# Performance work log

Measured on AMD Instinct MI355X. Metric: run time of the kernel, lower is better.

The kernel has to match this reference:

```python
import jax, jax.numpy as jnp
import numpy as np

B, T, V, E, H = 4096, 16, 512, 512, 1024


def setup_inputs() -> dict:
    key = jax.random.key(0)
    ks = jax.random.split(key, 8)
    s = 0.05  # weight init scale
    return {
        "encoded_input": jax.random.normal(ks[0], (B, H), jnp.float32),
        "target": jax.random.randint(ks[1], (B, T), 0, V, jnp.int32),
        "emb": jax.random.normal(ks[2], (V, E), jnp.float32) * s,
        "W_ih": jax.random.normal(ks[3], (4 * H, E), jnp.float32) * s,
        "W_hh": jax.random.normal(ks[4], (4 * H, H), jnp.float32) * s,
        "b_ih": jax.random.normal(ks[5], (4 * H,), jnp.float32) * s,
        "b_hh": jax.random.normal(ks[6], (4 * H,), jnp.float32) * s,
        "W_out": jax.random.normal(ks[7], (V, H), jnp.float32) * s,
    }


def reference(encoded_input, target, emb, W_ih, W_hh, b_ih, b_hh, W_out):
    # Teacher-forced char LSTM decoder. Dropout(0.1) is identity in eval mode.
    b, t = target.shape
    # input char ids: start token 0, then shifted targets
    inp_ids = jnp.concatenate(
        [jnp.zeros((b, 1), target.dtype), target[:, :-1]], axis=1)  # [B,T]
    x = emb[inp_ids]  # [B,T,E]
    # precompute input contribution to gates for all steps
    xg = jnp.einsum('bte,ge->btg', x, W_ih) + b_ih + b_hh  # [B,T,4H]

    def step(carry, xs):
        h, c = carry
        xg_t, tgt_t = xs  # [B,4H], [B]
        gates = xg_t + h @ W_hh.T  # [B,4H]
        i, f, g, o = jnp.split(gates, 4, axis=-1)  # torch order i,f,g,o
        i = jax.nn.sigmoid(i)
        f = jax.nn.sigmoid(f)
        g = jnp.tanh(g)
        o = jax.nn.sigmoid(o)
        c = f * c + i * g
        h = o * jnp.tanh(c)
        logits = h @ W_out.T  # [B,V]
        # NLL of log_softmax at target index, expressed stably
        lse = jax.nn.logsumexp(logits, axis=-1)
        tgt_logit = jnp.take_along_axis(logits, tgt_t[:, None], axis=1)[:, 0]
        loss_t = lse - tgt_logit  # [B]
        return (h, c), loss_t

    h0 = encoded_input  # hidden = (encoded, encoded) for 1 layer
    (_, _), losses = jax.lax.scan(
        step, (h0, h0),
        (jnp.swapaxes(xg, 0, 1), target.T))  # scan over time: [T,B,...]
    return losses.sum(axis=0) / t  # [B] per-example mean loss
```

## Files before the change

kernel.cpp:

```cpp
#include <hip/hip_runtime.h>
#include <hip/hip_bf16.h>
#include <stdint.h>

typedef __attribute__((ext_vector_type(8))) short bf16x8;
typedef __attribute__((ext_vector_type(4))) float f32x4;

#define DEV __device__ __forceinline__
#define MFMA16(a, b, c) __builtin_amdgcn_mfma_f32_16x16x32_bf16(a, b, c, 0, 0, 0)

static constexpr int Bn = 4096;
static constexpr int Tn = 16;
static constexpr int Vn = 512;
static constexpr int En = 512;
static constexpr int Hn = 1024;
static constexpr int G4 = 4096;

DEV unsigned short f2bf(float f) {
    union { float f; uint32_t u; } v; v.f = f;
    return (unsigned short)((v.u + 0x7fffu + ((v.u >> 16) & 1u)) >> 16);
}
DEV float bf2f(unsigned short h) {
    union { uint32_t u; float f; } v; v.u = (uint32_t)h << 16; return v.f;
}
DEV float sigmoidf_(float x) { return 1.f / (1.f + __expf(-x)); }
DEV float tanhf_(float x)    { return 1.f - 2.f / (1.f + __expf(2.f * x)); }

DEV bf16x8 cvt8(const float* p) {
    f32x4 a = *(const f32x4*)p;
    f32x4 b = *(const f32x4*)(p + 4);
    bf16x8 o;
    o[0] = (short)f2bf(a[0]); o[1] = (short)f2bf(a[1]);
    o[2] = (short)f2bf(a[2]); o[3] = (short)f2bf(a[3]);
    o[4] = (short)f2bf(b[0]); o[5] = (short)f2bf(b[1]);
    o[6] = (short)f2bf(b[2]); o[7] = (short)f2bf(b[3]);
    return o;
}

#define GLOAD16(s, d) __builtin_amdgcn_global_load_lds( \
    (const __attribute__((address_space(1))) uint32_t*)(s), \
    (__attribute__((address_space(3))) uint32_t*)(d), 16, 0, 0)

__launch_bounds__(1024, 4)
__global__ void lstm8(const unsigned short* __restrict__ Whp8,
                      const unsigned short* __restrict__ Hin,
                      const unsigned short* __restrict__ EGb,
                      const int* __restrict__ target, int t,
                      unsigned short* __restrict__ CstF,
                      unsigned short* __restrict__ Hout)
{
    __shared__ __align__(16) unsigned short lds[65536];

    const int tid = threadIdx.x;
    const int l   = tid & 63;
    const int w   = tid >> 6;
    const int wm  = w >> 2, wn = w & 3;
    const int q   = l >> 4, c15 = l & 15;
    const int bx  = blockIdx.x, by = blockIdx.y;
    const int n0  = bx * 256;
    const int U0  = by * 64;

    const int cBt = (((tid & 7) ^ ((tid >> 3) & 7)) << 3);
    const int sw0   = ((q ^ (c15 & 7)) << 3);
    const int offA0 = wm * 4096 + c15 * 64 + sw0;
    const int offB0 = wn * 4096 + c15 * 64 + sw0;

    f32x4 acc[4][4];
#pragma unroll
    for (int i = 0; i < 4; i++)
#pragma unroll
        for (int j = 0; j < 4; j++) acc[i][j] = f32x4{0.f, 0.f, 0.f, 0.f};

    auto stA = [&](int kts, int cbuf) {
        const unsigned short* page =
            Whp8 + (((size_t)(by * 16 + kts) * 2) << 13);
#pragma unroll
        for (int h = 0; h < 2; h++)
            GLOAD16(page + h * 8192 + tid * 8,
                    &lds[cbuf * 16384 + h * 8192 + tid * 8]);
    };
    auto stB = [&](int kts, int cbuf) {
#pragma unroll
        for (int h = 0; h < 2; h++)
            GLOAD16(Hin + (size_t)(n0 + h * 128 + (tid >> 3)) * Hn
                        + kts * 64 + cBt,
                    &lds[32768 + cbuf * 16384 + h * 8192 + tid * 8]);
    };

    stA(0, 0); stB(0, 0);
    stA(1, 1); stB(1, 1);
    asm volatile("s_waitcnt vmcnt(4)" ::: "memory");
    __builtin_amdgcn_s_barrier();

#pragma unroll 2
    for (int kt = 0; kt < 16; kt++) {
        const int cur = kt & 1;
        const unsigned short* Ab = &lds[cur * 16384];
        const unsigned short* Bb = &lds[32768 + cur * 16384];
        bf16x8 aF[4], bF[4];

#pragma unroll
        for (int i = 0; i < 4; i++)
            aF[i] = *(const bf16x8*)&Ab[offA0 + i * 1024];
#pragma unroll
        for (int j = 0; j < 4; j++)
            bF[j] = *(const bf16x8*)&Bb[offB0 + j * 1024];
        __builtin_amdgcn_s_setprio(1);
#pragma unroll
        for (int i = 0; i < 4; i++)
#pragma unroll
            for (int j = 0; j < 4; j++)
                acc[i][j] = MFMA16(aF[i], bF[j], acc[i][j]);
        __builtin_amdgcn_s_setprio(0);

#pragma unroll
        for (int i = 0; i < 4; i++)
            aF[i] = *(const bf16x8*)&Ab[(offA0 ^ 32) + i * 1024];
#pragma unroll
        for (int j = 0; j < 4; j++)
            bF[j] = *(const bf16x8*)&Bb[(offB0 ^ 32) + j * 1024];
        __builtin_amdgcn_s_setprio(1);
#pragma unroll
        for (int i = 0; i < 4; i++)
#pragma unroll
            for (int j = 0; j < 4; j++)
                acc[i][j] = MFMA16(aF[i], bF[j], acc[i][j]);
        __builtin_amdgcn_s_setprio(0);
        __builtin_amdgcn_s_barrier();

        const int kts = (kt + 2 < 16) ? (kt + 2) : 15;
        stA(kts, cur);
        stB(kts, cur);
        asm volatile("s_waitcnt vmcnt(4)" ::: "memory");
        __builtin_amdgcn_s_barrier();
    }

    int ids[4];
#pragma unroll
    for (int j = 0; j < 4; j++)
        ids[j] = (t > 0)
            ? target[(size_t)(n0 + wn * 64 + j * 16 + c15) * Tn + (t - 1)] : 0;

    unsigned short* sH = &lds[32768];
#pragma unroll
    for (int i = 0; i < 4; i++) {
        const int Uloc = wm * 16 + i * 4 + q;
#pragma unroll
        for (int j = 0; j < 4; j++) {
            uint2 egu = *(const uint2*)&EGb[(size_t)ids[j] * G4 + (U0 + Uloc) * 4];
            float e0 = bf2f((unsigned short)(egu.x & 0xffffu));
            float e1 = bf2f((unsigned short)(egu.x >> 16));
            float e2 = bf2f((unsigned short)(egu.y & 0xffffu));
            float e3 = bf2f((unsigned short)(egu.y >> 16));
            float ig = sigmoidf_(acc[i][j][0] + e0);
            float fg = sigmoidf_(acc[i][j][1] + e1);
            float gg = tanhf_  (acc[i][j][2] + e2);
            float og = sigmoidf_(acc[i][j][3] + e3);
            const size_t cidx =
                ((((size_t)(by * 16 + bx) * 16 + w) * 16 + i * 4 + j) << 6) + l;
            float cOld = bf2f(CstF[cidx]);
            float cNew = fg * cOld + ig * gg;
            float h    = og * tanhf_(cNew);
            CstF[cidx] = f2bf(cNew);
            const int bl = wn * 64 + j * 16 + c15;
            sH[bl * 64 + (Uloc ^ ((bl & 7) << 3))] = f2bf(h);
        }
    }
    __syncthreads();
    {
        const int row  = tid >> 2;
        const int part = tid & 3;
        size_t go = (size_t)(n0 + row) * Hn + U0;
#pragma unroll
        for (int s = 0; s < 2; s++) {
            const int slog = part * 2 + s;
            bf16x8 v = *(const bf16x8*)&sH[row * 64 + ((slog ^ (row & 7)) << 3)];
            *(bf16x8*)&Hout[go + slog * 8] = v;
        }
    }
}

__launch_bounds__(512, 1)
__global__ void logits256(const unsigned short* __restrict__ A,
                          const unsigned short* __restrict__ Wob,
                          const int* __restrict__ target,
                          float* __restrict__ partS,
                          float* __restrict__ partT)
{
    __shared__ __align__(16) unsigned short lds[65536];
    __shared__ float redS[4 * 256];
    __shared__ float redT[4 * 256];
    __shared__ int   tgL[256];

    const int tid = threadIdx.x;
    const int l   = tid & 63;
    const int w   = tid >> 6;
    const int wm  = w >> 2, wn = w & 3;
    const int q   = l >> 4, c15 = l & 15;
    const int bid = blockIdx.x;
    const int rb  = bid & 255, cb = bid >> 8;
    const int r0  = rb * 256;
    const int v0  = cb * 256;

    if (tid < 256) {
        int ra = r0 + tid;
        tgL[tid] = target[(size_t)(ra & (Bn - 1)) * Tn + (ra >> 12)];
    }

    const int cB    = (((l & 7) ^ (l >> 3)) << 3);
    const int sw0   = ((q ^ (c15 & 7)) << 3);
    const int offA0 = c15 * 64 + sw0;
    const int offB0 = ((wn & 1) * 64 + c15) * 64 + sw0;

    f32x4 acc[8][4];
#pragma unroll
    for (int i = 0; i < 8; i++)
#pragma unroll
        for (int j = 0; j < 4; j++) acc[i][j] = f32x4{0.f, 0.f, 0.f, 0.f};

    auto stA = [&](int kts, int cbuf) {
#pragma unroll
        for (int h = 0; h < 2; h++)
#pragma unroll
            for (int L = 0; L < 2; L++)
                GLOAD16(A + (size_t)(r0 + h * 128 + L * 64 + w * 8 + (l >> 3)) * Hn
                            + kts * 64 + cB,
                        &lds[cbuf * 16384 + h * 8192 + L * 4096 + w * 512]);
    };
    auto stB = [&](int kts, int cbuf) {
#pragma unroll
        for (int h = 0; h < 2; h++)
#pragma unroll
            for (int L = 0; L < 2; L++)
                GLOAD16(Wob + (size_t)(v0 + h * 128 + L * 64 + w * 8 + (l >> 3)) * Hn
                            + kts * 64 + cB,
                        &lds[32768 + cbuf * 16384 + h * 8192 + L * 4096 + w * 512]);
    };

    stA(0, 0); stB(0, 0);
    stA(1, 1); stB(1, 1);
    asm volatile("s_waitcnt vmcnt(8)" ::: "memory");
    __builtin_amdgcn_s_barrier();

#pragma unroll 2
    for (int kt = 0; kt < 16; kt++) {
        const int cur = kt & 1;
        const unsigned short* Ab = &lds[cur * 16384 + wm * 8192];
        const unsigned short* Bb = &lds[32768 + cur * 16384 + (wn >> 1) * 8192];
        bf16x8 aF[8], bF[4];

#pragma unroll
        for (int i = 0; i < 8; i++)
            aF[i] = *(const bf16x8*)&Ab[offA0 + i * 1024];
#pragma unroll
        for (int j = 0; j < 4; j++)
            bF[j] = *(const bf16x8*)&Bb[offB0 + j * 1024];
        __builtin_amdgcn_s_setprio(1);
#pragma unroll
        for (int i = 0; i < 8; i++)
#pragma unroll
            for (int j = 0; j < 4; j++)
                acc[i][j] = MFMA16(aF[i], bF[j], acc[i][j]);
        __builtin_amdgcn_s_setprio(0);

#pragma unroll
        for (int i = 0; i < 8; i++)
            aF[i] = *(const bf16x8*)&Ab[(offA0 ^ 32) + i * 1024];
#pragma unroll
        for (int j = 0; j < 4; j++)
            bF[j] = *(const bf16x8*)&Bb[(offB0 ^ 32) + j * 1024];
        __builtin_amdgcn_s_setprio(1);
#pragma unroll
        for (int i = 0; i < 8; i++)
#pragma unroll
            for (int j = 0; j < 4; j++)
                acc[i][j] = MFMA16(aF[i], bF[j], acc[i][j]);
        __builtin_amdgcn_s_setprio(0);
        __builtin_amdgcn_s_barrier();

        const int kts = (kt + 2 < 16) ? (kt + 2) : 15;
        stA(kts, cur);
        stB(kts, cur);
        asm volatile("s_waitcnt vmcnt(8)" ::: "memory");
        __builtin_amdgcn_s_barrier();
    }

#pragma unroll
    for (int i = 0; i < 8; i++)
#pragma unroll
        for (int rr = 0; rr < 4; rr++) {
            const int rloc = wm * 128 + i * 16 + q * 4 + rr;
            const int tg = tgL[rloc];
            float ps = 0.f, tv = 0.f;
#pragma unroll
            for (int j = 0; j < 4; j++) {
                float v = acc[i][j][rr];
                ps += __expf(v);
                int col = v0 + wn * 64 + j * 16 + c15;
                tv += (col == tg) ? v : 0.f;
            }
#pragma unroll
            for (int d = 1; d < 16; d <<= 1) {
                ps += __shfl_xor(ps, d);
                tv += __shfl_xor(tv, d);
            }
            if (c15 == 0) {
                redS[wn * 256 + rloc] = ps;
                redT[wn * 256 + rloc] = tv;
            }
        }
    __syncthreads();
    if (tid < 256) {
        float se = 0.f, tv = 0.f;
#pragma unroll
        for (int k = 0; k < 4; k++) {
            se += redS[k * 256 + tid];
            tv += redT[k * 256 + tid];
        }
        partS[(size_t)cb * (Bn * Tn) + r0 + tid] = se;
        partT[(size_t)cb * (Bn * Tn) + r0 + tid] = tv;
    }
}

template <int BM, int BN, int EPI>
__launch_bounds__(256, 2)
__global__ void gemm_k(const unsigned short* __restrict__ A, int lda,
                       const unsigned short* __restrict__ Bw, int ldb,
                       int K,
                       const float* __restrict__ biasp,
                       float* __restrict__ Out,
                       unsigned short* __restrict__ Outb, int ldo)
{
    constexpr int BK = 32;
    constexpr int WM = BM / 2, WN = BN / 2;
    constexpr int MI = WM / 16, NJ = WN / 16;

    __shared__ __align__(16) unsigned short sA[BM * BK];
    __shared__ __align__(16) unsigned short sB[BN * BK];

    const int tid = threadIdx.x;
    const int l   = tid & 63;
    const int w   = tid >> 6;
    const int wm  = w >> 1, wn = w & 1;
    const int m0  = blockIdx.y * BM;
    const int n0  = blockIdx.x * BN;

    f32x4 acc[MI][NJ];
#pragma unroll
    for (int i = 0; i < MI; i++)
#pragma unroll
        for (int j = 0; j < NJ; j++) acc[i][j] = f32x4{0.f, 0.f, 0.f, 0.f};

    const int srow = l >> 2;
    const int scol = (l & 3) * 8;
    const int q    = l >> 4;
    const int c15  = l & 15;

    for (int k0 = 0; k0 < K; k0 += BK) {
#pragma unroll
        for (int c = 0; c < BM / 64; c++)
            GLOAD16(A + (size_t)(m0 + c * 64 + w * 16 + srow) * lda + k0 + scol,
                    &sA[(c * 64 + w * 16) * BK]);
#pragma unroll
        for (int c = 0; c < BN / 64; c++)
            GLOAD16(Bw + (size_t)(n0 + c * 64 + w * 16 + srow) * ldb + k0 + scol,
                    &sB[(c * 64 + w * 16) * BK]);
        __syncthreads();

        bf16x8 aF[MI], bF[NJ];
#pragma unroll
        for (int i = 0; i < MI; i++)
            aF[i] = *(const bf16x8*)&sA[(wm * WM + i * 16 + c15) * BK + q * 8];
#pragma unroll
        for (int j = 0; j < NJ; j++)
            bF[j] = *(const bf16x8*)&sB[(wn * WN + j * 16 + c15) * BK + q * 8];
#pragma unroll
        for (int i = 0; i < MI; i++)
#pragma unroll
            for (int j = 0; j < NJ; j++)
                acc[i][j] = MFMA16(aF[i], bF[j], acc[i][j]);
        __syncthreads();
    }

#pragma unroll
    for (int j = 0; j < NJ; j++) {
        const int colp = n0 + wn * WN + j * 16 + c15;
        const float bj = biasp ? biasp[colp] : 0.f;
#pragma unroll
        for (int i = 0; i < MI; i++) {
            const size_t rb = (size_t)(m0 + wm * WM + i * 16 + 4 * q);
#pragma unroll
            for (int r = 0; r < 4; r++) {
                float vv = acc[i][j][r] + bj;
                if constexpr (EPI == 0) Out[(rb + r) * ldo + colp] = vv;
                else Outb[(rb + r) * ldo + colp] = f2bf(vv);
            }
        }
    }
}

__global__ void prep_all(const float* __restrict__ Wih,
                         const float* __restrict__ Whh,
                         const float* __restrict__ bih,
                         const float* __restrict__ bhh,
                         const float* __restrict__ Wout,
                         const float* __restrict__ emb,
                         unsigned short* __restrict__ Wihp,
                         unsigned short* __restrict__ Whp8,
                         float* __restrict__ biasp,
                         unsigned short* __restrict__ Wob,
                         unsigned short* __restrict__ embb)
{
    const int b = blockIdx.x;
    if (b < 1024) {
        int i = b * 256 + threadIdx.x;
        int n = i >> 6, kc = (i & 63) * 8;
        int g = n & 3, u = n >> 2;
        *(bf16x8*)&Wihp[(size_t)n * En + kc] =
            cvt8(Wih + (size_t)(g * Hn + u) * En + kc);
    } else if (b < 3072) {
        int idx = (b - 1024) * 256 + threadIdx.x;
        int o = idx * 8;
        int p = o & 8191;
        int h = (o >> 13) & 1;
        int kt = (o >> 14) & 15;
        int by = o >> 18;
        int r = p >> 6;
        int slot = (p & 63) >> 3;
        int cl = ((slot ^ (r & 7)) << 3);
        int n = by * 256 + h * 128 + r;
        int g = n & 3, u = n >> 2;
        *(bf16x8*)&Whp8[o] =
            cvt8(Whh + (size_t)(g * Hn + u) * Hn + kt * 64 + cl);
    } else if (b < 3088) {
        int n = (b - 3072) * 256 + threadIdx.x;
        int g = n & 3, u = n >> 2;
        biasp[n] = bih[g * Hn + u] + bhh[g * Hn + u];
    } else if (b < 3344) {
        int i = (b - 3088) * 256 + threadIdx.x;
        size_t off = (size_t)i * 8;
        *(bf16x8*)&Wob[off] = cvt8(Wout + off);
    } else {
        int i = (b - 3344) * 256 + threadIdx.x;
        size_t off = (size_t)i * 8;
        *(bf16x8*)&embb[off] = cvt8(emb + off);
    }
}

__global__ void init_state(const float* __restrict__ enc,
                           unsigned short* __restrict__ CstF,
                           unsigned short* __restrict__ Xh0,
                           float* __restrict__ loss)
{
    int f = blockIdx.x * 256 + threadIdx.x;
    int l = f & 63, q = l >> 4, c15 = l & 15;
    int ij = (f >> 6) & 15, i = ij >> 2, j = ij & 3;
    int w = (f >> 10) & 15, wm = w >> 2, wn = w & 3;
    int bx = (f >> 14) & 15, by = (f >> 18) & 15;
    int b = bx * 256 + wn * 64 + j * 16 + c15;
    int U = by * 64 + wm * 16 + i * 4 + q;
    CstF[f] = f2bf(enc[(size_t)b * Hn + U]);
    if (f < Bn * Hn / 8) {
        int m = f >> 7, u8 = (f & 127) * 8;
        *(bf16x8*)&Xh0[(size_t)m * Hn + u8] = cvt8(enc + (size_t)m * Hn + u8);
    }
    if (f < Bn) loss[f] = 0.f;
}

__global__ void lse_k(const unsigned short* __restrict__ lg,
                      const int* __restrict__ target, int t,
                      float* __restrict__ lossOut)
{
    int w = threadIdx.x >> 6, l = threadIdx.x & 63;
    int ra = blockIdx.x * 4 + w;
    const unsigned short* row = lg + (size_t)ra * Vn;
    bf16x8 v = *(const bf16x8*)&row[l * 8];
    float x0 = bf2f((unsigned short)v[0]), x1 = bf2f((unsigned short)v[1]);
    float x2 = bf2f((unsigned short)v[2]), x3 = bf2f((unsigned short)v[3]);
    float x4 = bf2f((unsigned short)v[4]), x5 = bf2f((unsigned short)v[5]);
    float x6 = bf2f((unsigned short)v[6]), x7 = bf2f((unsigned short)v[7]);
    float mx = fmaxf(fmaxf(fmaxf(x0, x1), fmaxf(x2, x3)),
                     fmaxf(fmaxf(x4, x5), fmaxf(x6, x7)));
#pragma unroll
    for (int d = 1; d < 64; d <<= 1) mx = fmaxf(mx, __shfl_xor(mx, d));
    float se = __expf(x0 - mx) + __expf(x1 - mx) + __expf(x2 - mx) +
               __expf(x3 - mx) + __expf(x4 - mx) + __expf(x5 - mx) +
               __expf(x6 - mx) + __expf(x7 - mx);
#pragma unroll
    for (int d = 1; d < 64; d <<= 1) se += __shfl_xor(se, d);
    if (l == 0) {
        int tg = target[(size_t)ra * Tn + t];
        lossOut[ra] += (mx + __logf(se)) - bf2f(row[tg]);
    }
}

__global__ void finalize_p(const float* __restrict__ partS,
                           const float* __restrict__ partT,
                           float* __restrict__ out)
{
    int m = blockIdx.x * 256 + threadIdx.x;
    float s = 0.f;
#pragma unroll
    for (int k = 0; k < 16; k++) {
        size_t ra = (size_t)k * Bn + m;
        float se = partS[ra] + partS[(size_t)(Bn * Tn) + ra];
        float tv = partT[ra] + partT[(size_t)(Bn * Tn) + ra];
        s += __logf(se) - tv;
    }
    out[m] = s * (1.f / 16.f);
}

__global__ void finalize_s(const float* __restrict__ loss,
                           float* __restrict__ out)
{
    int m = blockIdx.x * 256 + threadIdx.x;
    out[m] = loss[m] * (1.f / 16.f);
}

extern "C" void kernel_launch(void* const* d_in, const int* in_sizes, int n_in,
                              void* d_out, int out_size, void* d_ws, size_t ws_size,
                              hipStream_t stream)
{
    const float* enc    = (const float*)d_in[0];
    const int*   target = (const int*)d_in[1];
    const float* emb    = (const float*)d_in[2];
    const float* Wih    = (const float*)d_in[3];
    const float* Whh    = (const float*)d_in[4];
    const float* bih    = (const float*)d_in[5];
    const float* bhh    = (const float*)d_in[6];
    const float* Wout   = (const float*)d_in[7];
    float* out = (float*)d_out;
    (void)in_sizes; (void)n_in; (void)out_size;

    constexpr size_t SZ_Wihp  = (size_t)G4 * En * 2;
    constexpr size_t SZ_Whp8  = (size_t)G4 * Hn * 2;
    constexpr size_t SZ_Wob   = (size_t)Vn * Hn * 2;
    constexpr size_t SZ_biasp = (size_t)G4 * 4;
    constexpr size_t SZ_embb  = (size_t)Vn * En * 2;
    constexpr size_t SZ_EGb   = (size_t)Vn * G4 * 2;
    constexpr size_t SZ_Cst   = (size_t)Bn * Hn * 2;
    constexpr size_t SZ_H     = (size_t)Bn * Hn * 2;
    constexpr size_t SZ_LGS   = (size_t)Bn * Vn * 2;
    constexpr size_t SZ_PART  = (size_t)2 * Bn * Tn * 4;
    auto pad = [](size_t b) { return (b + 255) & ~(size_t)255; };
    const size_t fixed = pad(SZ_Wihp) + pad(SZ_Whp8) + pad(SZ_Wob) +
                         pad(SZ_biasp) + pad(SZ_embb) + pad(SZ_EGb) +
                         pad(SZ_Cst);
    const size_t needB = fixed + 17 * pad(SZ_H) + pad(SZ_LGS) +
                         2 * pad(SZ_PART);
    const bool batched = ws_size >= needB;

    size_t off = 0;
    char* base = (char*)d_ws;
    auto alloc = [&](size_t bytes) -> void* {
        void* p = base + off; off += pad(bytes); return p;
    };
    unsigned short* Wihp  = (unsigned short*)alloc(SZ_Wihp);
    unsigned short* Whp8  = (unsigned short*)alloc(SZ_Whp8);
    unsigned short* Wob   = (unsigned short*)alloc(SZ_Wob);
    float*          biasp = (float*)alloc(SZ_biasp);
    unsigned short* embb  = (unsigned short*)alloc(SZ_embb);
    unsigned short* EGb   = (unsigned short*)alloc(SZ_EGb);
    unsigned short* CstF  = (unsigned short*)alloc(SZ_Cst);
    const int nslot = batched ? 17 : 3;
    unsigned short* Hs    = (unsigned short*)alloc((size_t)nslot * pad(SZ_H));
    unsigned short* lgS   = (unsigned short*)alloc(SZ_LGS);
    float*          partS = (float*)alloc(SZ_PART);
    float*          partT = (float*)alloc(SZ_PART);
    const size_t HSLOT = pad(SZ_H) / 2;

    prep_all  <<<3472, 256, 0, stream>>>(Wih, Whh, bih, bhh, Wout, emb,
                                         Wihp, Whp8, biasp, Wob, embb);
    init_state<<<16384, 256, 0, stream>>>(enc, CstF, Hs, partS);

    gemm_k<128, 128, 2><<<dim3(32, 4), 256, 0, stream>>>(
        embb, En, Wihp, En, En, biasp, nullptr, EGb, G4);

    if (batched) {
        for (int t = 0; t < Tn; t++)
            lstm8<<<dim3(16, 16), 1024, 0, stream>>>(
                Whp8, Hs + (size_t)t * HSLOT, EGb, target, t, CstF,
                Hs + (size_t)(t + 1) * HSLOT);
        logits256<<<512, 512, 0, stream>>>(
            Hs + HSLOT, Wob, target, partS, partT);
        finalize_p<<<16, 256, 0, stream>>>(partS, partT, out);
    } else {
        for (int t = 0; t < Tn; t++) {
            unsigned short* hIn  = Hs + (size_t)(t % 3) * HSLOT;
            unsigned short* hOut = Hs + (size_t)((t + 1) % 3) * HSLOT;
            lstm8<<<dim3(16, 16), 1024, 0, stream>>>(
                Whp8, hIn, EGb, target, t, CstF, hOut);
            gemm_k<128, 64, 2><<<dim3(8, 32), 256, 0, stream>>>(
                hOut, Hn, Wob, Hn, Hn, nullptr, nullptr, lgS, Vn);
            lse_k<<<1024, 256, 0, stream>>>(lgS, target, t, partS);
        }
        finalize_s<<<16, 256, 0, stream>>>(partS, out);
    }
}
```

Measured before the change: 840.1 us.

## Retile LSTM step kernel to 256x128 blocks with plain row-major weights

Replaces the 1024-thread LSTM recurrence kernel (256x256 tile, K step 64, swizzled pre-paged weights) with a 512-thread kernel using a 256-gate by 128-batch tile and K step 32. It uses a simple row-major bf16 copy of W_hh, drops the XOR swizzle, and shrinks LDS from 128KB to 48KB so more blocks can be resident, with twice as many blocks in the grid. The cell-state layout in init and the weight prep are updated to match. The unswizzled LDS reads may cause bank conflicts, and the smaller K step doubles the barrier count per step.

```diff
diff --git a/kernel.cpp b/kernel.cpp
--- a/kernel.cpp
+++ b/kernel.cpp
@@ -40,29 +40,27 @@
     (const __attribute__((address_space(1))) uint32_t*)(s), \
     (__attribute__((address_space(3))) uint32_t*)(d), 16, 0, 0)
 
-__launch_bounds__(1024, 4)
-__global__ void lstm8(const unsigned short* __restrict__ Whp8,
-                      const unsigned short* __restrict__ Hin,
-                      const unsigned short* __restrict__ EGb,
-                      const int* __restrict__ target, int t,
-                      unsigned short* __restrict__ CstF,
-                      unsigned short* __restrict__ Hout)
-{
-    __shared__ __align__(16) unsigned short lds[65536];
+__launch_bounds__(512, 4)
+__global__ void lstm32(const unsigned short* __restrict__ Whp,
+                       const unsigned short* __restrict__ Hin,
+                       const unsigned short* __restrict__ EGb,
+                       const int* __restrict__ target, int t,
+                       unsigned short* __restrict__ CstF,
+                       unsigned short* __restrict__ Hout)
+{
+    __shared__ __align__(16) unsigned short lds[24576];
 
     const int tid = threadIdx.x;
     const int l   = tid & 63;
     const int w   = tid >> 6;
-    const int wm  = w >> 2, wn = w & 3;
+    const int wm  = w >> 1, wn = w & 1;
     const int q   = l >> 4, c15 = l & 15;
     const int bx  = blockIdx.x, by = blockIdx.y;
-    const int n0  = bx * 256;
+    const int n0  = bx * 128;
     const int U0  = by * 64;
 
-    const int cBt = (((tid & 7) ^ ((tid >> 3) & 7)) << 3);
-    const int sw0   = ((q ^ (c15 & 7)) << 3);
-    const int offA0 = wm * 4096 + c15 * 64 + sw0;
-    const int offB0 = wn * 4096 + c15 * 64 + sw0;
+    const int srow = tid >> 2;
+    const int scol = (tid & 3) * 8;
 
     f32x4 acc[4][4];
 #pragma unroll
@@ -71,53 +69,35 @@
         for (int j = 0; j < 4; j++) acc[i][j] = f32x4{0.f, 0.f, 0.f, 0.f};
 
     auto stA = [&](int kts, int cbuf) {
-        const unsigned short* page =
-            Whp8 + (((size_t)(by * 16 + kts) * 2) << 13);
-#pragma unroll
-        for (int h = 0; h < 2; h++)
-            GLOAD16(page + h * 8192 + tid * 8,
-                    &lds[cbuf * 16384 + h * 8192 + tid * 8]);
+#pragma unroll
+        for (int R = 0; R < 2; R++)
+            GLOAD16(Whp + (size_t)(by * 256 + R * 128 + srow) * Hn
+                        + kts * 32 + scol,
+                    &lds[cbuf * 8192 + R * 4096 + tid * 8]);
     };
     auto stB = [&](int kts, int cbuf) {
-#pragma unroll
-        for (int h = 0; h < 2; h++)
-            GLOAD16(Hin + (size_t)(n0 + h * 128 + (tid >> 3)) * Hn
-                        + kts * 64 + cBt,
-                    &lds[32768 + cbuf * 16384 + h * 8192 + tid * 8]);
+        GLOAD16(Hin + (size_t)(n0 + srow) * Hn + kts * 32 + scol,
+                &lds[16384 + cbuf * 4096 + tid * 8]);
     };
 
     stA(0, 0); stB(0, 0);
     stA(1, 1); stB(1, 1);
-    asm volatile("s_waitcnt vmcnt(4)" ::: "memory");
+    asm volatile("s_waitcnt vmcnt(3)" ::: "memory");
     __builtin_amdgcn_s_barrier();
 
 #pragma unroll 2
-    for (int kt = 0; kt < 16; kt++) {
+    for (int kt = 0; kt < 32; kt++) {
         const int cur = kt & 1;
-        const unsigned short* Ab = &lds[cur * 16384];
-        const unsigned short* Bb = &lds[32768 + cur * 16384];
+        const unsigned short* Ab = &lds[cur * 8192];
+        const unsigned short* Bb = &lds[16384 + cur * 4096];
         bf16x8 aF[4], bF[4];
 
 #pragma unroll
         for (int i = 0; i < 4; i++)
-            aF[i] = *(const bf16x8*)&Ab[offA0 + i * 1024];
+            aF[i] = *(const bf16x8*)&Ab[(wm * 64 + i * 16 + c15) * 32 + q * 8];
 #pragma unroll
         for (int j = 0; j < 4; j++)
-            bF[j] = *(const bf16x8*)&Bb[offB0 + j * 1024];
-        __builtin_amdgcn_s_setprio(1);
-#pragma unroll
-        for (int i = 0; i < 4; i++)
-#pragma unroll
-            for (int j = 0; j < 4; j++)
-                acc[i][j] = MFMA16(aF[i], bF[j], acc[i][j]);
-        __builtin_amdgcn_s_setprio(0);
-
-#pragma unroll
-        for (int i = 0; i < 4; i++)
-            aF[i] = *(const bf16x8*)&Ab[(offA0 ^ 32) + i * 1024];
-#pragma unroll
-        for (int j = 0; j < 4; j++)
-            bF[j] = *(const bf16x8*)&Bb[(offB0 ^ 32) + j * 1024];
+            bF[j] = *(const bf16x8*)&Bb[(wn * 64 + j * 16 + c15) * 32 + q * 8];
         __builtin_amdgcn_s_setprio(1);
 #pragma unroll
         for (int i = 0; i < 4; i++)
@@ -127,10 +107,10 @@
         __builtin_amdgcn_s_setprio(0);
         __builtin_amdgcn_s_barrier();
 
-        const int kts = (kt + 2 < 16) ? (kt + 2) : 15;
+        const int kts = (kt + 2 < 32) ? (kt + 2) : 31;
         stA(kts, cur);
         stB(kts, cur);
-        asm volatile("s_waitcnt vmcnt(4)" ::: "memory");
+        asm volatile("s_waitcnt vmcnt(3)" ::: "memory");
         __builtin_amdgcn_s_barrier();
     }
 
@@ -140,7 +120,7 @@
         ids[j] = (t > 0)
             ? target[(size_t)(n0 + wn * 64 + j * 16 + c15) * Tn + (t - 1)] : 0;
 
-    unsigned short* sH = &lds[32768];
+    unsigned short* sH = &lds[0];
 #pragma unroll
     for (int i = 0; i < 4; i++) {
         const int Uloc = wm * 16 + i * 4 + q;
@@ -156,7 +136,7 @@
             float gg = tanhf_  (acc[i][j][2] + e2);
             float og = sigmoidf_(acc[i][j][3] + e3);
             const size_t cidx =
-                ((((size_t)(by * 16 + bx) * 16 + w) * 16 + i * 4 + j) << 6) + l;
+                ((((size_t)(by * 32 + bx) * 8 + w) * 16 + i * 4 + j) << 6) + l;
             float cOld = bf2f(CstF[cidx]);
             float cNew = fg * cOld + ig * gg;
             float h    = og * tanhf_(cNew);
@@ -405,7 +385,7 @@
                          const float* __restrict__ Wout,
                          const float* __restrict__ emb,
                          unsigned short* __restrict__ Wihp,
-                         unsigned short* __restrict__ Whp8,
+                         unsigned short* __restrict__ Whp,
                          float* __restrict__ biasp,
                          unsigned short* __restrict__ Wob,
                          unsigned short* __restrict__ embb)
@@ -420,17 +400,9 @@
     } else if (b < 3072) {
         int idx = (b - 1024) * 256 + threadIdx.x;
         int o = idx * 8;
-        int p = o & 8191;
-        int h = (o >> 13) & 1;
-        int kt = (o >> 14) & 15;
-        int by = o >> 18;
-        int r = p >> 6;
-        int slot = (p & 63) >> 3;
-        int cl = ((slot ^ (r & 7)) << 3);
-        int n = by * 256 + h * 128 + r;
+        int n = o >> 10, kc = o & 1023;
         int g = n & 3, u = n >> 2;
-        *(bf16x8*)&Whp8[o] =
-            cvt8(Whh + (size_t)(g * Hn + u) * Hn + kt * 64 + cl);
+        *(bf16x8*)&Whp[o] = cvt8(Whh + (size_t)(g * Hn + u) * Hn + kc);
     } else if (b < 3088) {
         int n = (b - 3072) * 256 + threadIdx.x;
         int g = n & 3, u = n >> 2;
@@ -454,9 +426,9 @@
     int f = blockIdx.x * 256 + threadIdx.x;
     int l = f & 63, q = l >> 4, c15 = l & 15;
     int ij = (f >> 6) & 15, i = ij >> 2, j = ij & 3;
-    int w = (f >> 10) & 15, wm = w >> 2, wn = w & 3;
-    int bx = (f >> 14) & 15, by = (f >> 18) & 15;
-    int b = bx * 256 + wn * 64 + j * 16 + c15;
+    int w = (f >> 10) & 7, wm = w >> 1, wn = w & 1;
+    int bx = (f >> 13) & 31, by = (f >> 18) & 15;
+    int b = bx * 128 + wn * 64 + j * 16 + c15;
     int U = by * 64 + wm * 16 + i * 4 + q;
     CstF[f] = f2bf(enc[(size_t)b * Hn + U]);
     if (f < Bn * Hn / 8) {
@@ -532,7 +504,7 @@
     (void)in_sizes; (void)n_in; (void)out_size;
 
     constexpr size_t SZ_Wihp  = (size_t)G4 * En * 2;
-    constexpr size_t SZ_Whp8  = (size_t)G4 * Hn * 2;
+    constexpr size_t SZ_Whp   = (size_t)G4 * Hn * 2;
     constexpr size_t SZ_Wob   = (size_t)Vn * Hn * 2;
     constexpr size_t SZ_biasp = (size_t)G4 * 4;
     constexpr size_t SZ_embb  = (size_t)Vn * En * 2;
@@ -542,7 +514,7 @@
     constexpr size_t SZ_LGS   = (size_t)Bn * Vn * 2;
     constexpr size_t SZ_PART  = (size_t)2 * Bn * Tn * 4;
     auto pad = [](size_t b) { return (b + 255) & ~(size_t)255; };
-    const size_t fixed = pad(SZ_Wihp) + pad(SZ_Whp8) + pad(SZ_Wob) +
+    const size_t fixed = pad(SZ_Wihp) + pad(SZ_Whp) + pad(SZ_Wob) +
                          pad(SZ_biasp) + pad(SZ_embb) + pad(SZ_EGb) +
                          pad(SZ_Cst);
     const size_t needB = fixed + 17 * pad(SZ_H) + pad(SZ_LGS) +
@@ -555,7 +527,7 @@
         void* p = base + off; off += pad(bytes); return p;
     };
     unsigned short* Wihp  = (unsigned short*)alloc(SZ_Wihp);
-    unsigned short* Whp8  = (unsigned short*)alloc(SZ_Whp8);
+    unsigned short* Whp   = (unsigned short*)alloc(SZ_Whp);
     unsigned short* Wob   = (unsigned short*)alloc(SZ_Wob);
     float*          biasp = (float*)alloc(SZ_biasp);
     unsigned short* embb  = (unsigned short*)alloc(SZ_embb);
@@ -569,7 +541,7 @@
     const size_t HSLOT = pad(SZ_H) / 2;
 
     prep_all  <<<3472, 256, 0, stream>>>(Wih, Whh, bih, bhh, Wout, emb,
-                                         Wihp, Whp8, biasp, Wob, embb);
+                                         Wihp, Whp, biasp, Wob, embb);
     init_state<<<16384, 256, 0, stream>>>(enc, CstF, Hs, partS);
 
     gemm_k<128, 128, 2><<<dim3(32, 4), 256, 0, stream>>>(
@@ -577,8 +549,8 @@
 
     if (batched) {
         for (int t = 0; t < Tn; t++)
-            lstm8<<<dim3(16, 16), 1024, 0, stream>>>(
-                Whp8, Hs + (size_t)t * HSLOT, EGb, target, t, CstF,
+            lstm32<<<dim3(32, 16), 512, 0, stream>>>(
+                Whp, Hs + (size_t)t * HSLOT, EGb, target, t, CstF,
                 Hs + (size_t)(t + 1) * HSLOT);
         logits256<<<512, 512, 0, stream>>>(
             Hs + HSLOT, Wob, target, partS, partT);
@@ -587,8 +559,8 @@
         for (int t = 0; t < Tn; t++) {
             unsigned short* hIn  = Hs + (size_t)(t % 3) * HSLOT;
             unsigned short* hOut = Hs + (size_t)((t + 1) % 3) * HSLOT;
-            lstm8<<<dim3(16, 16), 1024, 0, stream>>>(
-                Whp8, hIn, EGb, target, t, CstF, hOut);
+            lstm32<<<dim3(32, 16), 512, 0, stream>>>(
+                Whp, hIn, EGb, target, t, CstF, hOut);
             gemm_k<128, 64, 2><<<dim3(8, 32), 256, 0, stream>>>(
                 hOut, Hn, Wob, Hn, Hn, nullptr, nullptr, lgS, Vn);
             lse_k<<<1024, 256, 0, stream>>>(lgS, target, t, partS);
```

New measurement: 873.4 us. 1.04x slower.
